# Kernel tuning notes

Hardware: AMD Instinct MI355X
Metric: run time of the kernel (lower is better)

## Reference

```python
import jax, jax.numpy as jnp
import numpy as np

B, K, H, W = 32, 8, 512, 512
S = 50              # n_samples = min(50, H*W*K)
HID = 64
CTX = 9 * K - 1     # 71


def setup_inputs() -> dict:
    key = jax.random.key(0)
    ks = jax.random.split(key, 6)
    # binary latent code grid
    z = jax.random.randint(ks[0], (B, K, H, W), 0, 2).astype(jnp.float32)
    # pre-sampled (bit, row, col) picks replacing the torch.randint loop
    b_idx = jax.random.randint(ks[1], (S,), 0, K, dtype=jnp.int32)
    i_idx = jax.random.randint(ks[2], (S,), 0, H, dtype=jnp.int32)
    j_idx = jax.random.randint(ks[3], (S,), 0, W, dtype=jnp.int32)
    # predictor MLP params (torch Linear: y = x @ W^T + b; we store [in,out])
    W1 = jax.random.normal(ks[4], (CTX, HID), jnp.float32) / np.sqrt(CTX).astype(np.float32)
    b1 = jnp.zeros((HID,), jnp.float32)
    W2 = jax.random.normal(ks[5], (HID, 1), jnp.float32) / np.sqrt(HID).astype(np.float32)
    b2 = jnp.zeros((1,), jnp.float32)
    return dict(z=z, W1=W1, b1=b1, W2=W2, b2=b2,
                b_idx=b_idx, i_idx=i_idx, j_idx=j_idx)


def reference(z, W1, b1, W2, b2, b_idx, i_idx, j_idx):
    Bq, Kq, Hq, Wq = z.shape
    Sq = b_idx.shape[0]
    # 3x3 toroidal neighborhood offsets, ordered (di major, dj minor) as in torch loop
    offs = jnp.array([-1, 0, 1], dtype=jnp.int32)
    di = jnp.repeat(offs, 3)   # [9]
    dj = jnp.tile(offs, 3)     # [9]
    ni = (i_idx[:, None] + di[None, :]) % Hq   # [S,9]
    nj = (j_idx[:, None] + dj[None, :]) % Wq   # [S,9]
    # gather all 9 neighbors for all K bits: [B,K,S,9]
    g = z[:, :, ni, nj]
    # torch ordering: for (di,dj) in 9 neighbors, for b in range(K) -> neighbor-major, bit-minor
    full = jnp.transpose(g, (0, 2, 3, 1)).reshape(Bq, Sq, 9 * Kq)   # [B,S,72]
    # drop the center bit itself (neighbor index 4 = (0,0), bit b_idx)
    rm = 4 * Kq + b_idx                         # [S]
    t = jnp.arange(9 * Kq - 1, dtype=jnp.int32) # [71]
    idx = t[None, :] + (t[None, :] >= rm[:, None]).astype(jnp.int32)  # [S,71]
    ctx = jnp.take_along_axis(full, idx[None, :, :], axis=2)         # [B,S,71]
    # tiny 2-layer MLP, batched over all samples at once
    h = jax.nn.relu(ctx @ W1 + b1)              # [B,S,64]
    logit = (h @ W2 + b2)[..., 0]               # [B,S]
    pred = (logit > 0).astype(z.dtype)
    actual = z[:, b_idx, i_idx, j_idx]          # [B,S]
    # per-sample mean over batch, then mean over samples == global mean
    return jnp.mean((pred != actual).astype(jnp.float32))
```

## Files before the change

### kernel.cpp

```cpp
#include <hip/hip_runtime.h>

#define BB 32
#define KK 8
#define HH 512
#define WW 512
#define SS 50
#define HID 64
#define CTX 71

#define NPB  4
#define TPB  (NPB * 64)
#define NBLK (BB * SS / NPB)
#define RTPB 128

__global__ void __launch_bounds__(TPB)
le_core_kernel(const float* __restrict__ z,
               const float* __restrict__ W1,
               const float* __restrict__ b1,
               const float* __restrict__ W2,
               const float* __restrict__ b2,
               const int*   __restrict__ b_idx,
               const int*   __restrict__ i_idx,
               const int*   __restrict__ j_idx,
               float*       __restrict__ partial)
{
    const int wave = threadIdx.x >> 6;
    const int lane = threadIdx.x & 63;
    const int bs   = blockIdx.x * NPB + wave;
    const int b    = bs / SS;
    const int s    = bs - b * SS;

    __shared__ float sW1[CTX * HID];
    __shared__ float sFull[NPB][9 * KK];
    __shared__ float sflag[NPB];

    const int i0 = i_idx[s];
    const int j0 = j_idx[s];
    const int rm = 4 * KK + b_idx[s];

    {
        const int n  = lane >> 3;
        const int k  = lane & 7;
        const int ni = (i0 + (n / 3) - 1) & (HH - 1);
        const int nj = (j0 + (n % 3) - 1) & (WW - 1);
        sFull[wave][lane] = z[(((b * KK + k) * HH + ni) * WW) + nj];
    }
    if (lane < 8) {
        const int ni = (i0 + 1) & (HH - 1);
        const int nj = (j0 + 1) & (WW - 1);
        sFull[wave][64 + lane] = z[(((b * KK + lane) * HH + ni) * WW) + nj];
    }

    {
        const float4* s4 = (const float4*)W1;
        float4*       d4 = (float4*)sW1;
        for (int idx = threadIdx.x; idx < (CTX * HID) / 4; idx += TPB)
            d4[idx] = s4[idx];
    }
    __syncthreads();

    float acc = b1[lane];
    #pragma unroll
    for (int t = 0; t < CTX; ++t) {
        const int src = t + (t >= rm ? 1 : 0);
        acc = fmaf(sFull[wave][src], sW1[t * HID + lane], acc);
    }
    const float hv      = acc > 0.0f ? acc : 0.0f;
    float       contrib = hv * W2[lane];

    #pragma unroll
    for (int off = 32; off > 0; off >>= 1)
        contrib += __shfl_down(contrib, off);

    if (lane == 0) {
        const float logit = contrib + b2[0];
        const float pred  = logit > 0.0f ? 1.0f : 0.0f;
        sflag[wave] = (pred != sFull[wave][rm]) ? 1.0f : 0.0f;
    }
    __syncthreads();

    if (threadIdx.x == 0)
        partial[blockIdx.x] = sflag[0] + sflag[1] + sflag[2] + sflag[3];
}

__global__ void __launch_bounds__(RTPB)
le_reduce_kernel(const float* __restrict__ partial, float* __restrict__ out)
{
    const int tid = threadIdx.x;
    float ssum = 0.0f;
    for (int i = tid; i < NBLK; i += RTPB) ssum += partial[i];

    #pragma unroll
    for (int off = 32; off > 0; off >>= 1)
        ssum += __shfl_down(ssum, off);

    __shared__ float wsum[RTPB / 64];
    if ((tid & 63) == 0) wsum[tid >> 6] = ssum;
    __syncthreads();
    if (tid == 0)
        out[0] = (wsum[0] + wsum[1]) * (1.0f / (float)(BB * SS));
}

extern "C" void kernel_launch(void* const* d_in, const int* in_sizes, int n_in,
                              void* d_out, int out_size, void* d_ws, size_t ws_size,
                              hipStream_t stream)
{
    const float* z     = (const float*)d_in[0];
    const float* W1    = (const float*)d_in[1];
    const float* b1    = (const float*)d_in[2];
    const float* W2    = (const float*)d_in[3];
    const float* b2    = (const float*)d_in[4];
    const int*   b_idx = (const int*)d_in[5];
    const int*   i_idx = (const int*)d_in[6];
    const int*   j_idx = (const int*)d_in[7];

    float* out     = (float*)d_out;
    float* partial = (float*)d_ws;

    le_core_kernel<<<NBLK, TPB, 0, stream>>>(z, W1, b1, W2, b2,
                                             b_idx, i_idx, j_idx, partial);
    le_reduce_kernel<<<1, RTPB, 0, stream>>>(partial, out);
}
```

Before: 11.70 us.

## Bit-pack binary context via wave ballots and double samples per block

Context values are binary, so the neighbor gather now goes into registers, gets packed into a 72-bit mask with wave ballots, and the center bit is removed with 128-bit shifts. Each matmul term then becomes a conditional add of the W1 weight instead of an FMA that reads the shared-memory context array. Blocks now hold 8 samples instead of 4, which halves the number of blocks that copy W1 into shared memory. The reduce kernel shrinks to a single wave doing float4 loads. This relies on z being exactly 0/1 (it thresholds at 0.5), and the larger blocks lower the block count and so the parallelism.

```diff
diff --git a/kernel.cpp b/kernel.cpp
--- a/kernel.cpp
+++ b/kernel.cpp
@@ -8,10 +8,9 @@
 #define HID 64
 #define CTX 71
 
-#define NPB  4
+#define NPB  8
 #define TPB  (NPB * 64)
 #define NBLK (BB * SS / NPB)
-#define RTPB 128
 
 __global__ void __launch_bounds__(TPB)
 le_core_kernel(const float* __restrict__ z,
@@ -31,39 +30,57 @@
     const int s    = bs - b * SS;
 
     __shared__ float sW1[CTX * HID];
-    __shared__ float sFull[NPB][9 * KK];
     __shared__ float sflag[NPB];
 
     const int i0 = i_idx[s];
     const int j0 = j_idx[s];
     const int rm = 4 * KK + b_idx[s];
 
+    float z0, z1 = 0.0f;
     {
         const int n  = lane >> 3;
         const int k  = lane & 7;
         const int ni = (i0 + (n / 3) - 1) & (HH - 1);
         const int nj = (j0 + (n % 3) - 1) & (WW - 1);
-        sFull[wave][lane] = z[(((b * KK + k) * HH + ni) * WW) + nj];
+        z0 = z[(((b * KK + k) * HH + ni) * WW) + nj];
     }
     if (lane < 8) {
         const int ni = (i0 + 1) & (HH - 1);
         const int nj = (j0 + 1) & (WW - 1);
-        sFull[wave][64 + lane] = z[(((b * KK + lane) * HH + ni) * WW) + nj];
+        z1 = z[(((b * KK + lane) * HH + ni) * WW) + nj];
     }
 
     {
         const float4* s4 = (const float4*)W1;
         float4*       d4 = (float4*)sW1;
+        #pragma unroll
         for (int idx = threadIdx.x; idx < (CTX * HID) / 4; idx += TPB)
             d4[idx] = s4[idx];
     }
+
+    const unsigned long long mlo = __ballot(z0 > 0.5f);
+    const unsigned long long mhi = __ballot(z1 > 0.5f) & 0xFFull;
+
+    const float actual = (float)((unsigned)(mlo >> rm) & 1u);
+
+    const unsigned __int128 M  = ((unsigned __int128)mhi << 64) | mlo;
+    const unsigned __int128 lo = M & ((((unsigned __int128)1) << rm) - 1);
+    const unsigned __int128 C  = lo | ((M >> (rm + 1)) << rm);
+    const unsigned long long clo = (unsigned long long)C;
+    const unsigned long long chi = (unsigned long long)(C >> 64);
+
     __syncthreads();
 
     float acc = b1[lane];
     #pragma unroll
-    for (int t = 0; t < CTX; ++t) {
-        const int src = t + (t >= rm ? 1 : 0);
-        acc = fmaf(sFull[wave][src], sW1[t * HID + lane], acc);
+    for (int t = 0; t < 64; ++t) {
+        const float wv = sW1[t * HID + lane];
+        acc += ((clo >> t) & 1ull) ? wv : 0.0f;
+    }
+    #pragma unroll
+    for (int t = 64; t < CTX; ++t) {
+        const float wv = sW1[t * HID + lane];
+        acc += ((chi >> (t - 64)) & 1ull) ? wv : 0.0f;
     }
     const float hv      = acc > 0.0f ? acc : 0.0f;
     float       contrib = hv * W2[lane];
@@ -75,30 +92,32 @@
     if (lane == 0) {
         const float logit = contrib + b2[0];
         const float pred  = logit > 0.0f ? 1.0f : 0.0f;
-        sflag[wave] = (pred != sFull[wave][rm]) ? 1.0f : 0.0f;
+        sflag[wave] = (pred != actual) ? 1.0f : 0.0f;
     }
     __syncthreads();
 
-    if (threadIdx.x == 0)
-        partial[blockIdx.x] = sflag[0] + sflag[1] + sflag[2] + sflag[3];
+    if (threadIdx.x == 0) {
+        float blk = 0.0f;
+        #pragma unroll
+        for (int w = 0; w < NPB; ++w) blk += sflag[w];
+        partial[blockIdx.x] = blk;
+    }
 }
 
-__global__ void __launch_bounds__(RTPB)
+__global__ void __launch_bounds__(64)
 le_reduce_kernel(const float* __restrict__ partial, float* __restrict__ out)
 {
     const int tid = threadIdx.x;
-    float ssum = 0.0f;
-    for (int i = tid; i < NBLK; i += RTPB) ssum += partial[i];
+    float4 v = make_float4(0.f, 0.f, 0.f, 0.f);
+    if (tid < NBLK / 4)
+        v = ((const float4*)partial)[tid];
+    float ssum = (v.x + v.y) + (v.z + v.w);
 
     #pragma unroll
     for (int off = 32; off > 0; off >>= 1)
         ssum += __shfl_down(ssum, off);
 
-    __shared__ float wsum[RTPB / 64];
-    if ((tid & 63) == 0) wsum[tid >> 6] = ssum;
-    __syncthreads();
-    if (tid == 0)
-        out[0] = (wsum[0] + wsum[1]) * (1.0f / (float)(BB * SS));
+    if (tid == 0) out[0] = ssum * (1.0f / (float)(BB * SS));
 }
 
 extern "C" void kernel_launch(void* const* d_in, const int* in_sizes, int n_in,
@@ -119,5 +138,5 @@
 
     le_core_kernel<<<NBLK, TPB, 0, stream>>>(z, W1, b1, W2, b2,
                                              b_idx, i_idx, j_idx, partial);
-    le_reduce_kernel<<<1, RTPB, 0, stream>>>(partial, out);
+    le_reduce_kernel<<<1, 64, 0, stream>>>(partial, out);
 }
```

New measurement: 10.91 us. 1.07x faster.
